# Kernel optimization log

Hardware: AMD Instinct MI355X
Metric: run time of the kernel (lower is better)

The kernel has to match this reference:

```python
import jax, jax.numpy as jnp
import numpy as np

FEAT = 1024
B = 1024
S = 64


def setup_inputs() -> dict:
    key = jax.random.key(0)
    ks = jax.random.split(key, 6)
    scale_ih = 1.0 / np.sqrt(2 * FEAT)
    scale_hh = 1.0 / np.sqrt(FEAT)
    return {
        "query": jax.random.normal(ks[0], (B, FEAT), jnp.float32) * 0.1,
        "support_context": jax.random.normal(ks[1], (S, FEAT), jnp.float32) * 0.1,
        "W_ih": jax.random.normal(ks[2], (4 * FEAT, 2 * FEAT), jnp.float32) * scale_ih,
        "W_hh": jax.random.normal(ks[3], (4 * FEAT, FEAT), jnp.float32) * scale_hh,
        "b_ih": jax.random.normal(ks[4], (4 * FEAT,), jnp.float32) * scale_hh,
        "b_hh": jax.random.normal(ks[5], (4 * FEAT,), jnp.float32) * scale_hh,
    }


def reference(query, support_context, W_ih, W_hh, b_ih, b_hh):
    # query: [B, F]; support_context: [S, F]; steps == S
    hidden = query
    cell = jnp.zeros_like(query)
    support_t = support_context.T  # [F, S]

    def step(carry, _):
        h, c = carry
        attn = jax.nn.softmax(h @ support_t, axis=1)          # [B, S]
        readout = attn @ support_context                      # [B, F]
        x = jnp.concatenate([query, readout], axis=1)         # [B, 2F]
        gates = x @ W_ih.T + b_ih + h @ W_hh.T + b_hh          # [B, 4F]
        i, f, g, o = jnp.split(gates, 4, axis=1)               # torch LSTMCell gate order
        c_new = jax.nn.sigmoid(f) * c + jax.nn.sigmoid(i) * jnp.tanh(g)
        h_new = jax.nn.sigmoid(o) * jnp.tanh(c_new) + query   # skip connection per original
        return (h_new, c_new), None

    (hidden, cell), _ = jax.lax.scan(step, (hidden, cell), None,
                                     length=support_context.shape[0])
    return hidden
```

## Files before the change

### kernel.cpp

```cpp
#include <hip/hip_runtime.h>
#include <hip/hip_bf16.h>


typedef __attribute__((ext_vector_type(8))) __bf16 bf16x8;
typedef __attribute__((ext_vector_type(4))) float f32x4;
typedef __attribute__((ext_vector_type(8))) unsigned short ushort8;

__device__ __forceinline__ ushort f2bf(float f) {
  union { float f; unsigned int u; } v; v.f = f;
  unsigned int u = v.u;
  u += 0x7FFFu + ((u >> 16) & 1u);
  return (ushort)(u >> 16);
}
__device__ __forceinline__ float bf2f(ushort u) {
  union { float f; unsigned int u; } v; v.u = ((unsigned int)u) << 16; return v.f;
}
__device__ __forceinline__ float sigm_(float x) { return 1.f / (1.f + __expf(-x)); }
__device__ __forceinline__ float tanh_(float x) {
  x = fminf(15.f, fmaxf(-15.f, x));
  float e = __expf(2.f * x);
  return (e - 1.f) / (e + 1.f);
}
__device__ __forceinline__ void async16(ushort* lds, const ushort* g) {
  __builtin_amdgcn_global_load_lds(
      (const __attribute__((address_space(1))) void*)g,
      (__attribute__((address_space(3))) void*)lds, 16, 0, 0);
}
__device__ __forceinline__ int permrow(int n) {
  int g = n >> 10, j = n & 1023;
  return ((j >> 4) << 6) | (g << 4) | (j & 15);
}

__global__ __launch_bounds__(256) void prep_kernel(
    const float* __restrict__ query, const float* __restrict__ support,
    const float* __restrict__ W_ih, const float* __restrict__ W_hh,
    const float* __restrict__ b_ih, const float* __restrict__ b_hh,
    ushort* __restrict__ Wq_bf, ushort* __restrict__ Wcomb,
    float* __restrict__ bias_p, ushort* __restrict__ X0,
    float* __restrict__ c, float* __restrict__ sT,
    ushort* __restrict__ Wr_bf, ushort* __restrict__ Sb)
{
  int g = blockIdx.x * 256 + threadIdx.x;
  int n = g >> 10, k = g & 1023;
  int np = permrow(n);
  Wq_bf[(size_t)np * 1024 + k] = f2bf(W_ih[(size_t)n * 2048 + k]);
  Wr_bf[(size_t)n * 1024 + k]  = f2bf(W_ih[(size_t)n * 2048 + 1024 + k]);
  Wcomb[(size_t)np * 1088 + k] = f2bf(W_hh[(size_t)n * 1024 + k]);
  if (g < 1024 * 1024) {
    X0[(size_t)(g >> 10) * 1088 + (g & 1023)] = f2bf(query[g]);
    c[g] = 0.f;
  }
  if (g < 4096) bias_p[permrow(g)] = b_ih[g] + b_hh[g];
  if (g < 65536) {
    int kk = g >> 6, s = g & 63;
    float v = support[(size_t)s * 1024 + kk];
    sT[g] = v;
    Sb[(size_t)s * 1024 + kk] = f2bf(v);
  }
}

__global__ __launch_bounds__(256) void sw_mfma(
    const ushort* __restrict__ Wr, const ushort* __restrict__ Sb,
    ushort* __restrict__ Wcomb)
{
  __shared__ ushort As[3][128 * 32];
  __shared__ ushort Bs[3][64 * 32];
  const int t = threadIdx.x;
  const int bm0 = blockIdx.x * 128;
  const int w = t >> 6, l = t & 63;
  const int wm = w * 32;
  const int srow = t >> 2, scol = (t & 3) * 8;
  const ushort* ga0 = Wr + (size_t)(bm0 + srow) * 1024 + scol;
  const ushort* ga1 = Wr + (size_t)(bm0 + 64 + srow) * 1024 + scol;
  const ushort* gb0 = Sb + (size_t)srow * 1024 + scol;
  const int fr = l & 15, fk = (l >> 4) * 8, fq = l >> 4;
  f32x4 acc[2][4] = {};
  const int nt = 32;
  async16(&As[0][t * 8], ga0); async16(&As[0][2048 + t * 8], ga1);
  async16(&Bs[0][t * 8], gb0);
  async16(&As[1][t * 8], ga0 + 32); async16(&As[1][2048 + t * 8], ga1 + 32);
  async16(&Bs[1][t * 8], gb0 + 32);
  for (int it = 0; it < nt; it++) {
    if (it + 1 < nt) { asm volatile("s_waitcnt vmcnt(3)" ::: "memory"); }
    else             { asm volatile("s_waitcnt vmcnt(0)" ::: "memory"); }
    __builtin_amdgcn_s_barrier();
    __builtin_amdgcn_sched_barrier(0);
    const int b = it % 3;
    const ushort* pa = &As[b][(wm + fr) * 32 + fk];
    const ushort* pb = &Bs[b][fr * 32 + fk];
    bf16x8 af[2], bfv[4];
#pragma unroll
    for (int mi = 0; mi < 2; mi++) af[mi] = *(const bf16x8*)(pa + mi * 512);
#pragma unroll
    for (int ni = 0; ni < 4; ni++) bfv[ni] = *(const bf16x8*)(pb + ni * 512);
    if (it + 2 < nt) {
      const int pbuf = (it + 2) % 3;
      const int k0 = (it + 2) << 5;
      async16(&As[pbuf][t * 8], ga0 + k0); async16(&As[pbuf][2048 + t * 8], ga1 + k0);
      async16(&Bs[pbuf][t * 8], gb0 + k0);
    }
#pragma unroll
    for (int mi = 0; mi < 2; mi++)
#pragma unroll
      for (int ni = 0; ni < 4; ni++)
        acc[mi][ni] = __builtin_amdgcn_mfma_f32_16x16x32_bf16(af[mi], bfv[ni], acc[mi][ni], 0, 0, 0);
  }
#pragma unroll
  for (int mi = 0; mi < 2; mi++)
#pragma unroll
    for (int ni = 0; ni < 4; ni++) {
      int s = ni * 16 + fr;
      int row0 = bm0 + wm + mi * 16 + fq * 4;
#pragma unroll
      for (int jj = 0; jj < 4; jj++)
        Wcomb[(size_t)permrow(row0 + jj) * 1088 + 1024 + s] = f2bf(acc[mi][ni][jj]);
    }
}

__global__ __launch_bounds__(256) void attn_kernel(
    const ushort* __restrict__ Xh, const float* __restrict__ sT,
    ushort* __restrict__ Xa)
{
  __shared__ float hs[4][1024];
  __shared__ float part[4][4][64];
  int t = threadIdx.x;
  int b0 = blockIdx.x * 4;
#pragma unroll
  for (int i = 0; i < 2; i++) {
    int r = i * 2 + (t >> 7), c8 = (t & 127) << 3;
    ushort8 v = *(const ushort8*)&Xh[(size_t)(b0 + r) * 1088 + c8];
#pragma unroll
    for (int jj = 0; jj < 8; jj++) hs[r][c8 + jj] = bf2f(v[jj]);
  }
  __syncthreads();
  int s = t & 63, q = t >> 6;
  const float* st = sT + (size_t)q * 256 * 64 + s;
  const float* hp0 = &hs[0][q * 256];
  const float* hp1 = &hs[1][q * 256];
  const float* hp2 = &hs[2][q * 256];
  const float* hp3 = &hs[3][q * 256];
  float a0 = 0.f, a1 = 0.f, a2 = 0.f, a3 = 0.f;
#pragma unroll 4
  for (int kk = 0; kk < 256; kk += 4) {
    float s0 = st[(size_t)kk * 64], s1 = st[(size_t)(kk + 1) * 64];
    float s2 = st[(size_t)(kk + 2) * 64], s3 = st[(size_t)(kk + 3) * 64];
    float4 h0 = *(const float4*)&hp0[kk];
    float4 h1 = *(const float4*)&hp1[kk];
    float4 h2 = *(const float4*)&hp2[kk];
    float4 h3 = *(const float4*)&hp3[kk];
    a0 += h0.x * s0 + h0.y * s1 + h0.z * s2 + h0.w * s3;
    a1 += h1.x * s0 + h1.y * s1 + h1.z * s2 + h1.w * s3;
    a2 += h2.x * s0 + h2.y * s1 + h2.z * s2 + h2.w * s3;
    a3 += h3.x * s0 + h3.y * s1 + h3.z * s2 + h3.w * s3;
  }
  part[q][0][s] = a0; part[q][1][s] = a1; part[q][2][s] = a2; part[q][3][s] = a3;
  __syncthreads();
  {
    int r = t >> 6, s2 = t & 63;
    float v = part[0][r][s2] + part[1][r][s2] + part[2][r][s2] + part[3][r][s2];
    float m = v;
    for (int off = 32; off; off >>= 1) m = fmaxf(m, __shfl_xor(m, off));
    float e = __expf(v - m);
    float sm = e;
    for (int off = 32; off; off >>= 1) sm += __shfl_xor(sm, off);
    Xa[(size_t)(b0 + r) * 1088 + 1024 + s2] = f2bf(e / sm);
  }
}

__global__ __launch_bounds__(256) void gemm_step(
    const ushort* __restrict__ A, const ushort* __restrict__ Bw,
    int lda, int ldb, int K,
    const float* __restrict__ base, const float* __restrict__ bias,
    float* __restrict__ Cout,
    float* __restrict__ cbuf, const float* __restrict__ query,
    ushort* __restrict__ Xout, float* __restrict__ outp)
{
  __shared__ ushort As[3][2][64 * 32];
  __shared__ ushort Bs[3][2][128 * 32];
  const int t = threadIdx.x;
  const int bid = blockIdx.x;
  const int xcd = bid & 7, idx = bid >> 3;
  const int bx = idx & 15, byy = idx >> 4;
  const int by = xcd * 4 + byy;
  const int m0 = bx * 64, n0 = by * 128;
  const int w = t >> 6, l = t & 63;
  const int wm = (w >> 1) * 32, wn = (w & 1) * 64;
  const int srow = t >> 2, scol = (t & 3) * 8;
  const ushort* ga  = A  + (size_t)(m0 + srow) * lda + scol;
  const ushort* gb0 = Bw + (size_t)(n0 + srow) * ldb + scol;
  const ushort* gb1 = Bw + (size_t)(n0 + 64 + srow) * ldb + scol;
  const int fr = l & 15, fk = (l >> 4) * 8, fq = l >> 4;
  f32x4 acc[2][4] = {};
  const int nt = K >> 6;
#define STAGE(buf, k0)                                        \
  async16(&As[buf][0][t * 8], ga + (k0));                     \
  async16(&As[buf][1][t * 8], ga + (k0) + 32);                \
  async16(&Bs[buf][0][t * 8], gb0 + (k0));                    \
  async16(&Bs[buf][0][2048 + t * 8], gb1 + (k0));             \
  async16(&Bs[buf][1][t * 8], gb0 + (k0) + 32);               \
  async16(&Bs[buf][1][2048 + t * 8], gb1 + (k0) + 32);
  STAGE(0, 0)
  STAGE(1, 64)
  for (int it = 0; it < nt; it++) {
    if (it + 1 < nt) { asm volatile("s_waitcnt vmcnt(6)" ::: "memory"); }
    else             { asm volatile("s_waitcnt vmcnt(0)" ::: "memory"); }
    __builtin_amdgcn_s_barrier();
    __builtin_amdgcn_sched_barrier(0);
    if (it + 2 < nt) {
      const int pbuf = (it + 2) % 3;
      const int k0 = (it + 2) << 6;
      STAGE(pbuf, k0)
    }
    const int b = it % 3;
#pragma unroll
    for (int kk = 0; kk < 2; kk++) {
      const ushort* pa = &As[b][kk][(wm + fr) * 32 + fk];
      const ushort* pb = &Bs[b][kk][(wn + fr) * 32 + fk];
      bf16x8 af[2], bfv[4];
#pragma unroll
      for (int mi = 0; mi < 2; mi++) af[mi] = *(const bf16x8*)(pa + mi * 512);
#pragma unroll
      for (int ni = 0; ni < 4; ni++) bfv[ni] = *(const bf16x8*)(pb + ni * 512);
      __builtin_amdgcn_s_setprio(1);
#pragma unroll
      for (int mi = 0; mi < 2; mi++)
#pragma unroll
        for (int ni = 0; ni < 4; ni++)
          acc[mi][ni] = __builtin_amdgcn_mfma_f32_16x16x32_bf16(af[mi], bfv[ni], acc[mi][ni], 0, 0, 0);
      __builtin_amdgcn_s_setprio(0);
    }
  }
#undef STAGE
  if (!base) {
#pragma unroll
    for (int mi = 0; mi < 2; mi++)
#pragma unroll
      for (int ni = 0; ni < 4; ni++) {
        int col = n0 + wn + ni * 16 + fr;
        int row0 = m0 + wm + mi * 16 + fq * 4;
        float bv = bias[col];
#pragma unroll
        for (int jj = 0; jj < 4; jj++)
          Cout[(size_t)(row0 + jj) * 4096 + col] = acc[mi][ni][jj] + bv;
      }
    return;
  }
  const int jbase = (((n0 + wn) >> 6) << 4);
  const int jcol = jbase + fr;
#pragma unroll
  for (int mi = 0; mi < 2; mi++) {
#pragma unroll
    for (int jj = 0; jj < 4; jj++) {
      int row = m0 + wm + mi * 16 + fq * 4 + jj;
      const float* bp = base + (size_t)row * 4096 + (n0 + wn);
      float gi = acc[mi][0][jj] + bp[fr];
      float gf = acc[mi][1][jj] + bp[16 + fr];
      float gg = acc[mi][2][jj] + bp[32 + fr];
      float go = acc[mi][3][jj] + bp[48 + fr];
      size_t cidx = (size_t)row * 1024 + jcol;
      float cv = cbuf[cidx];
      float cn = sigm_(gf) * cv + sigm_(gi) * tanh_(gg);
      float hn = sigm_(go) * tanh_(cn) + query[cidx];
      cbuf[cidx] = cn;
      Xout[(size_t)row * 1088 + jcol] = f2bf(hn);
      if (outp) outp[cidx] = hn;
    }
  }
}

extern "C" void kernel_launch(void* const* d_in, const int* in_sizes, int n_in,
                              void* d_out, int out_size, void* d_ws, size_t ws_size,
                              hipStream_t stream) {
  const float* query   = (const float*)d_in[0];
  const float* support = (const float*)d_in[1];
  const float* W_ih    = (const float*)d_in[2];
  const float* W_hh    = (const float*)d_in[3];
  const float* b_ih    = (const float*)d_in[4];
  const float* b_hh    = (const float*)d_in[5];
  float* out = (float*)d_out;

  char* ws = (char*)d_ws;
  size_t off = 0;
  auto alloc = [&](size_t bytes) {
    void* p = ws + off;
    off += (bytes + 255) & ~(size_t)255;
    return p;
  };
  ushort* Wq_bf  = (ushort*)alloc((size_t)4096 * 1024 * 2);
  ushort* Wcomb  = (ushort*)alloc((size_t)4096 * 1088 * 2);
  ushort* Wr_bf  = (ushort*)alloc((size_t)4096 * 1024 * 2);
  ushort* Sb     = (ushort*)alloc((size_t)64 * 1024 * 2);
  float*  bias_p = (float*) alloc((size_t)4096 * 4);
  float*  base   = (float*) alloc((size_t)1024 * 4096 * 4);
  ushort* X0     = (ushort*)alloc((size_t)1024 * 1088 * 2);
  ushort* X1     = (ushort*)alloc((size_t)1024 * 1088 * 2);
  float*  c      = (float*) alloc((size_t)1024 * 1024 * 4);
  float*  sT     = (float*) alloc((size_t)1024 * 64 * 4);

  prep_kernel<<<16384, 256, 0, stream>>>(query, support, W_ih, W_hh, b_ih, b_hh,
                                         Wq_bf, Wcomb, bias_p, X0, c, sT,
                                         Wr_bf, Sb);
  sw_mfma<<<32, 256, 0, stream>>>(Wr_bf, Sb, Wcomb);
  gemm_step<<<512, 256, 0, stream>>>(X0, Wq_bf, 1088, 1024, 1024,
                                     nullptr, bias_p, base,
                                     nullptr, nullptr, nullptr, nullptr);
  for (int step = 0; step < 64; step++) {
    ushort* Xc = (step & 1) ? X1 : X0;
    ushort* Xn = (step & 1) ? X0 : X1;
    attn_kernel<<<256, 256, 0, stream>>>(Xc, sT, Xc);
    gemm_step<<<512, 256, 0, stream>>>(Xc, Wcomb, 1088, 1088, 1088,
                                       base, nullptr, nullptr,
                                       c, query, Xn,
                                       (step == 63) ? out : nullptr);
  }
}
```

Before: 2.014 ms.

## Fuse attention scores and softmax into the per-step LSTM gate GEMM

Removes the separate attention kernel. Each gate-GEMM block now computes h·S^T with extra MFMAs while it streams h tiles, does a softmax in LDS, and applies the attention-times-(W_r·S) term as a final K=64 chunk. This cuts one launch per step and the global round trip of the attention weights. In exchange, every block recomputes the attention scores for its 64 rows, which duplicates work across the 32 column blocks. The h buffer layout also shrinks to 1024 columns.

```diff
diff --git a/kernel.cpp b/kernel.cpp
--- a/kernel.cpp
+++ b/kernel.cpp
@@ -37,8 +37,8 @@
     const float* __restrict__ b_ih, const float* __restrict__ b_hh,
     ushort* __restrict__ Wq_bf, ushort* __restrict__ Wcomb,
     float* __restrict__ bias_p, ushort* __restrict__ X0,
-    float* __restrict__ c, float* __restrict__ sT,
-    ushort* __restrict__ Wr_bf, ushort* __restrict__ Sb)
+    float* __restrict__ c, ushort* __restrict__ Wr_bf,
+    ushort* __restrict__ Sb)
 {
   int g = blockIdx.x * 256 + threadIdx.x;
   int n = g >> 10, k = g & 1023;
@@ -47,16 +47,11 @@
   Wr_bf[(size_t)n * 1024 + k]  = f2bf(W_ih[(size_t)n * 2048 + 1024 + k]);
   Wcomb[(size_t)np * 1088 + k] = f2bf(W_hh[(size_t)n * 1024 + k]);
   if (g < 1024 * 1024) {
-    X0[(size_t)(g >> 10) * 1088 + (g & 1023)] = f2bf(query[g]);
+    X0[g] = f2bf(query[g]);
     c[g] = 0.f;
   }
   if (g < 4096) bias_p[permrow(g)] = b_ih[g] + b_hh[g];
-  if (g < 65536) {
-    int kk = g >> 6, s = g & 63;
-    float v = support[(size_t)s * 1024 + kk];
-    sT[g] = v;
-    Sb[(size_t)s * 1024 + kk] = f2bf(v);
-  }
+  if (g < 65536) Sb[g] = f2bf(support[g]);
 }
 
 __global__ __launch_bounds__(256) void sw_mfma(
@@ -117,61 +112,80 @@
     }
 }
 
-__global__ __launch_bounds__(256) void attn_kernel(
-    const ushort* __restrict__ Xh, const float* __restrict__ sT,
-    ushort* __restrict__ Xa)
+__global__ __launch_bounds__(256) void gemm_base(
+    const ushort* __restrict__ A, const ushort* __restrict__ Bw,
+    const float* __restrict__ bias, float* __restrict__ Cout)
 {
-  __shared__ float hs[4][1024];
-  __shared__ float part[4][4][64];
-  int t = threadIdx.x;
-  int b0 = blockIdx.x * 4;
-#pragma unroll
-  for (int i = 0; i < 2; i++) {
-    int r = i * 2 + (t >> 7), c8 = (t & 127) << 3;
-    ushort8 v = *(const ushort8*)&Xh[(size_t)(b0 + r) * 1088 + c8];
-#pragma unroll
-    for (int jj = 0; jj < 8; jj++) hs[r][c8 + jj] = bf2f(v[jj]);
-  }
-  __syncthreads();
-  int s = t & 63, q = t >> 6;
-  const float* st = sT + (size_t)q * 256 * 64 + s;
-  const float* hp0 = &hs[0][q * 256];
-  const float* hp1 = &hs[1][q * 256];
-  const float* hp2 = &hs[2][q * 256];
-  const float* hp3 = &hs[3][q * 256];
-  float a0 = 0.f, a1 = 0.f, a2 = 0.f, a3 = 0.f;
-#pragma unroll 4
-  for (int kk = 0; kk < 256; kk += 4) {
-    float s0 = st[(size_t)kk * 64], s1 = st[(size_t)(kk + 1) * 64];
-    float s2 = st[(size_t)(kk + 2) * 64], s3 = st[(size_t)(kk + 3) * 64];
-    float4 h0 = *(const float4*)&hp0[kk];
-    float4 h1 = *(const float4*)&hp1[kk];
-    float4 h2 = *(const float4*)&hp2[kk];
-    float4 h3 = *(const float4*)&hp3[kk];
-    a0 += h0.x * s0 + h0.y * s1 + h0.z * s2 + h0.w * s3;
-    a1 += h1.x * s0 + h1.y * s1 + h1.z * s2 + h1.w * s3;
-    a2 += h2.x * s0 + h2.y * s1 + h2.z * s2 + h2.w * s3;
-    a3 += h3.x * s0 + h3.y * s1 + h3.z * s2 + h3.w * s3;
-  }
-  part[q][0][s] = a0; part[q][1][s] = a1; part[q][2][s] = a2; part[q][3][s] = a3;
-  __syncthreads();
-  {
-    int r = t >> 6, s2 = t & 63;
-    float v = part[0][r][s2] + part[1][r][s2] + part[2][r][s2] + part[3][r][s2];
-    float m = v;
-    for (int off = 32; off; off >>= 1) m = fmaxf(m, __shfl_xor(m, off));
-    float e = __expf(v - m);
-    float sm = e;
-    for (int off = 32; off; off >>= 1) sm += __shfl_xor(sm, off);
-    Xa[(size_t)(b0 + r) * 1088 + 1024 + s2] = f2bf(e / sm);
-  }
-}
-
-__global__ __launch_bounds__(256) void gemm_step(
-    const ushort* __restrict__ A, const ushort* __restrict__ Bw,
-    int lda, int ldb, int K,
-    const float* __restrict__ base, const float* __restrict__ bias,
-    float* __restrict__ Cout,
+  __shared__ ushort As[3][2][64 * 32];
+  __shared__ ushort Bs[3][2][128 * 32];
+  const int t = threadIdx.x;
+  const int bid = blockIdx.x;
+  const int xcd = bid & 7, idx = bid >> 3;
+  const int bx = idx & 15, byy = idx >> 4;
+  const int by = xcd * 4 + byy;
+  const int m0 = bx * 64, n0 = by * 128;
+  const int w = t >> 6, l = t & 63;
+  const int wm = (w >> 1) * 32, wn = (w & 1) * 64;
+  const int srow = t >> 2, scol = (t & 3) * 8;
+  const ushort* ga  = A  + (size_t)(m0 + srow) * 1024 + scol;
+  const ushort* gb0 = Bw + (size_t)(n0 + srow) * 1024 + scol;
+  const ushort* gb1 = Bw + (size_t)(n0 + 64 + srow) * 1024 + scol;
+  const int fr = l & 15, fk = (l >> 4) * 8, fq = l >> 4;
+  f32x4 acc[2][4] = {};
+  const int nt = 16;
+#define BSTAGE(buf, k0)                                       \
+  async16(&As[buf][0][t * 8], ga + (k0));                     \
+  async16(&As[buf][1][t * 8], ga + (k0) + 32);                \
+  async16(&Bs[buf][0][t * 8], gb0 + (k0));                    \
+  async16(&Bs[buf][0][2048 + t * 8], gb1 + (k0));             \
+  async16(&Bs[buf][1][t * 8], gb0 + (k0) + 32);               \
+  async16(&Bs[buf][1][2048 + t * 8], gb1 + (k0) + 32);
+  BSTAGE(0, 0)
+  BSTAGE(1, 64)
+  for (int it = 0; it < nt; it++) {
+    if (it + 1 < nt) { asm volatile("s_waitcnt vmcnt(6)" ::: "memory"); }
+    else             { asm volatile("s_waitcnt vmcnt(0)" ::: "memory"); }
+    __builtin_amdgcn_s_barrier();
+    __builtin_amdgcn_sched_barrier(0);
+    if (it + 2 < nt) { const int pb = (it + 2) % 3; const int k0 = (it + 2) << 6; BSTAGE(pb, k0) }
+    const int b = it % 3;
+#pragma unroll
+    for (int kk = 0; kk < 2; kk++) {
+      const ushort* pa = &As[b][kk][(wm + fr) * 32 + fk];
+      const ushort* pb2 = &Bs[b][kk][(wn + fr) * 32 + fk];
+      bf16x8 af[2], bfv[4];
+#pragma unroll
+      for (int mi = 0; mi < 2; mi++) af[mi] = *(const bf16x8*)(pa + mi * 512);
+#pragma unroll
+      for (int ni = 0; ni < 4; ni++) bfv[ni] = *(const bf16x8*)(pb2 + ni * 512);
+      __builtin_amdgcn_s_setprio(1);
+#pragma unroll
+      for (int mi = 0; mi < 2; mi++)
+#pragma unroll
+        for (int ni = 0; ni < 4; ni++)
+          acc[mi][ni] = __builtin_amdgcn_mfma_f32_16x16x32_bf16(af[mi], bfv[ni], acc[mi][ni], 0, 0, 0);
+      __builtin_amdgcn_s_setprio(0);
+    }
+  }
+#undef BSTAGE
+#pragma unroll
+  for (int mi = 0; mi < 2; mi++)
+#pragma unroll
+    for (int ni = 0; ni < 4; ni++) {
+      int col = n0 + wn + ni * 16 + fr;
+      int row0 = m0 + wm + mi * 16 + fq * 4;
+      float bv = bias[col];
+#pragma unroll
+      for (int jj = 0; jj < 4; jj++)
+        Cout[(size_t)(row0 + jj) * 4096 + col] = acc[mi][ni][jj] + bv;
+    }
+}
+
+__global__ __launch_bounds__(256, 2) void gemm_fused(
+    const ushort* __restrict__ A,
+    const ushort* __restrict__ Wcomb,
+    const ushort* __restrict__ Sb,
+    const float* __restrict__ base,
     float* __restrict__ cbuf, const float* __restrict__ query,
     ushort* __restrict__ Xout, float* __restrict__ outp)
 {
@@ -186,67 +200,124 @@
   const int w = t >> 6, l = t & 63;
   const int wm = (w >> 1) * 32, wn = (w & 1) * 64;
   const int srow = t >> 2, scol = (t & 3) * 8;
-  const ushort* ga  = A  + (size_t)(m0 + srow) * lda + scol;
-  const ushort* gb0 = Bw + (size_t)(n0 + srow) * ldb + scol;
-  const ushort* gb1 = Bw + (size_t)(n0 + 64 + srow) * ldb + scol;
+  const ushort* ga  = A + (size_t)(m0 + srow) * 1024 + scol;
+  const ushort* gb0 = Wcomb + (size_t)(n0 + srow) * 1088 + scol;
+  const ushort* gb1 = Wcomb + (size_t)(n0 + 64 + srow) * 1088 + scol;
   const int fr = l & 15, fk = (l >> 4) * 8, fq = l >> 4;
+  const ushort* gsb = Sb + (size_t)((w & 1) * 32 + fr) * 1024 + fk;
   f32x4 acc[2][4] = {};
-  const int nt = K >> 6;
-#define STAGE(buf, k0)                                        \
+  f32x4 lacc[2][2] = {};
+#define FSTAGE_A(buf, k0)                                     \
   async16(&As[buf][0][t * 8], ga + (k0));                     \
-  async16(&As[buf][1][t * 8], ga + (k0) + 32);                \
+  async16(&As[buf][1][t * 8], ga + (k0) + 32);
+#define FSTAGE_B(buf, k0)                                     \
   async16(&Bs[buf][0][t * 8], gb0 + (k0));                    \
   async16(&Bs[buf][0][2048 + t * 8], gb1 + (k0));             \
   async16(&Bs[buf][1][t * 8], gb0 + (k0) + 32);               \
   async16(&Bs[buf][1][2048 + t * 8], gb1 + (k0) + 32);
-  STAGE(0, 0)
-  STAGE(1, 64)
-  for (int it = 0; it < nt; it++) {
-    if (it + 1 < nt) { asm volatile("s_waitcnt vmcnt(6)" ::: "memory"); }
-    else             { asm volatile("s_waitcnt vmcnt(0)" ::: "memory"); }
+  FSTAGE_A(0, 0) FSTAGE_B(0, 0)
+  FSTAGE_A(1, 64) FSTAGE_B(1, 64)
+  asm volatile("s_waitcnt vmcnt(6)" ::: "memory");
+  for (int it = 0; it < 16; it++) {
     __builtin_amdgcn_s_barrier();
     __builtin_amdgcn_sched_barrier(0);
-    if (it + 2 < nt) {
-      const int pbuf = (it + 2) % 3;
-      const int k0 = (it + 2) << 6;
-      STAGE(pbuf, k0)
-    }
+    const int k0 = it << 6;
+    bf16x8 sb00 = *(const bf16x8*)(gsb + k0);
+    bf16x8 sb01 = *(const bf16x8*)(gsb + k0 + 32);
+    bf16x8 sb10 = *(const bf16x8*)(gsb + k0 + 16384);
+    bf16x8 sb11 = *(const bf16x8*)(gsb + k0 + 16384 + 32);
+    if (it <= 13) { const int pb = (it + 2) % 3; FSTAGE_A(pb, k0 + 128) FSTAGE_B(pb, k0 + 128) }
+    else if (it == 14) { FSTAGE_B(1, 1024) }
     const int b = it % 3;
+    bf16x8 af2[2][2];
 #pragma unroll
     for (int kk = 0; kk < 2; kk++) {
       const ushort* pa = &As[b][kk][(wm + fr) * 32 + fk];
-      const ushort* pb = &Bs[b][kk][(wn + fr) * 32 + fk];
-      bf16x8 af[2], bfv[4];
-#pragma unroll
-      for (int mi = 0; mi < 2; mi++) af[mi] = *(const bf16x8*)(pa + mi * 512);
-#pragma unroll
-      for (int ni = 0; ni < 4; ni++) bfv[ni] = *(const bf16x8*)(pb + ni * 512);
+      const ushort* pb2 = &Bs[b][kk][(wn + fr) * 32 + fk];
+      bf16x8 bfv[4];
+#pragma unroll
+      for (int mi = 0; mi < 2; mi++) af2[kk][mi] = *(const bf16x8*)(pa + mi * 512);
+#pragma unroll
+      for (int ni = 0; ni < 4; ni++) bfv[ni] = *(const bf16x8*)(pb2 + ni * 512);
       __builtin_amdgcn_s_setprio(1);
 #pragma unroll
       for (int mi = 0; mi < 2; mi++)
 #pragma unroll
         for (int ni = 0; ni < 4; ni++)
-          acc[mi][ni] = __builtin_amdgcn_mfma_f32_16x16x32_bf16(af[mi], bfv[ni], acc[mi][ni], 0, 0, 0);
+          acc[mi][ni] = __builtin_amdgcn_mfma_f32_16x16x32_bf16(af2[kk][mi], bfv[ni], acc[mi][ni], 0, 0, 0);
       __builtin_amdgcn_s_setprio(0);
     }
-  }
-#undef STAGE
-  if (!base) {
+    if (it <= 13)      { asm volatile("s_waitcnt vmcnt(6)" ::: "memory"); }
+    else if (it == 14) { asm volatile("s_waitcnt vmcnt(4)" ::: "memory"); }
+    else               { asm volatile("s_waitcnt vmcnt(0)" ::: "memory"); }
+    __builtin_amdgcn_sched_barrier(0);
+    lacc[0][0] = __builtin_amdgcn_mfma_f32_16x16x32_bf16(af2[0][0], sb00, lacc[0][0], 0, 0, 0);
+    lacc[0][1] = __builtin_amdgcn_mfma_f32_16x16x32_bf16(af2[0][0], sb10, lacc[0][1], 0, 0, 0);
+    lacc[1][0] = __builtin_amdgcn_mfma_f32_16x16x32_bf16(af2[0][1], sb00, lacc[1][0], 0, 0, 0);
+    lacc[1][1] = __builtin_amdgcn_mfma_f32_16x16x32_bf16(af2[0][1], sb10, lacc[1][1], 0, 0, 0);
+    lacc[0][0] = __builtin_amdgcn_mfma_f32_16x16x32_bf16(af2[1][0], sb01, lacc[0][0], 0, 0, 0);
+    lacc[0][1] = __builtin_amdgcn_mfma_f32_16x16x32_bf16(af2[1][0], sb11, lacc[0][1], 0, 0, 0);
+    lacc[1][0] = __builtin_amdgcn_mfma_f32_16x16x32_bf16(af2[1][1], sb01, lacc[1][0], 0, 0, 0);
+    lacc[1][1] = __builtin_amdgcn_mfma_f32_16x16x32_bf16(af2[1][1], sb11, lacc[1][1], 0, 0, 0);
+  }
+  __builtin_amdgcn_s_barrier();
+  {
+    float* lg = (float*)&Bs[0][0][0];
+    const int sbase = (w & 1) * 32;
 #pragma unroll
     for (int mi = 0; mi < 2; mi++)
 #pragma unroll
-      for (int ni = 0; ni < 4; ni++) {
-        int col = n0 + wn + ni * 16 + fr;
-        int row0 = m0 + wm + mi * 16 + fq * 4;
-        float bv = bias[col];
+      for (int ni = 0; ni < 2; ni++) {
+        int s = sbase + ni * 16 + fr;
+        int r0 = wm + mi * 16 + fq * 4;
 #pragma unroll
         for (int jj = 0; jj < 4; jj++)
-          Cout[(size_t)(row0 + jj) * 4096 + col] = acc[mi][ni][jj] + bv;
+          lg[(r0 + jj) * 64 + s] = lacc[mi][ni][jj];
       }
-    return;
-  }
-  const int jbase = (((n0 + wn) >> 6) << 4);
-  const int jcol = jbase + fr;
+  }
+  __syncthreads();
+  {
+    const int r = t >> 2, q = t & 3;
+    float* lg = (float*)&Bs[0][0][0];
+    float p[16];
+#pragma unroll
+    for (int i = 0; i < 16; i++) p[i] = lg[r * 64 + q * 16 + i];
+    float mx = p[0];
+#pragma unroll
+    for (int i = 1; i < 16; i++) mx = fmaxf(mx, p[i]);
+    mx = fmaxf(mx, __shfl_xor(mx, 1));
+    mx = fmaxf(mx, __shfl_xor(mx, 2));
+    float sm = 0.f;
+#pragma unroll
+    for (int i = 0; i < 16; i++) { p[i] = __expf(p[i] - mx); sm += p[i]; }
+    sm += __shfl_xor(sm, 1);
+    sm += __shfl_xor(sm, 2);
+    float inv = 1.f / sm;
+    ushort* at = &As[1][q >> 1][r * 32 + (q & 1) * 16];
+#pragma unroll
+    for (int i = 0; i < 16; i++) at[i] = f2bf(p[i] * inv);
+  }
+  __syncthreads();
+#pragma unroll
+  for (int kk = 0; kk < 2; kk++) {
+    const ushort* pa = &As[1][kk][(wm + fr) * 32 + fk];
+    const ushort* pb2 = &Bs[1][kk][(wn + fr) * 32 + fk];
+    bf16x8 af[2], bfv[4];
+#pragma unroll
+    for (int mi = 0; mi < 2; mi++) af[mi] = *(const bf16x8*)(pa + mi * 512);
+#pragma unroll
+    for (int ni = 0; ni < 4; ni++) bfv[ni] = *(const bf16x8*)(pb2 + ni * 512);
+    __builtin_amdgcn_s_setprio(1);
+#pragma unroll
+    for (int mi = 0; mi < 2; mi++)
+#pragma unroll
+      for (int ni = 0; ni < 4; ni++)
+        acc[mi][ni] = __builtin_amdgcn_mfma_f32_16x16x32_bf16(af[mi], bfv[ni], acc[mi][ni], 0, 0, 0);
+    __builtin_amdgcn_s_setprio(0);
+  }
+#undef FSTAGE_A
+#undef FSTAGE_B
+  const int jcol = (((n0 + wn) >> 6) << 4) + fr;
 #pragma unroll
   for (int mi = 0; mi < 2; mi++) {
 #pragma unroll
@@ -262,7 +333,7 @@
       float cn = sigm_(gf) * cv + sigm_(gi) * tanh_(gg);
       float hn = sigm_(go) * tanh_(cn) + query[cidx];
       cbuf[cidx] = cn;
-      Xout[(size_t)row * 1088 + jcol] = f2bf(hn);
+      Xout[cidx] = f2bf(hn);
       if (outp) outp[cidx] = hn;
     }
   }
@@ -292,25 +363,19 @@
   ushort* Sb     = (ushort*)alloc((size_t)64 * 1024 * 2);
   float*  bias_p = (float*) alloc((size_t)4096 * 4);
   float*  base   = (float*) alloc((size_t)1024 * 4096 * 4);
-  ushort* X0     = (ushort*)alloc((size_t)1024 * 1088 * 2);
-  ushort* X1     = (ushort*)alloc((size_t)1024 * 1088 * 2);
+  ushort* X0     = (ushort*)alloc((size_t)1024 * 1024 * 2);
+  ushort* X1     = (ushort*)alloc((size_t)1024 * 1024 * 2);
   float*  c      = (float*) alloc((size_t)1024 * 1024 * 4);
-  float*  sT     = (float*) alloc((size_t)1024 * 64 * 4);
 
   prep_kernel<<<16384, 256, 0, stream>>>(query, support, W_ih, W_hh, b_ih, b_hh,
-                                         Wq_bf, Wcomb, bias_p, X0, c, sT,
-                                         Wr_bf, Sb);
+                                         Wq_bf, Wcomb, bias_p, X0, c, Wr_bf, Sb);
   sw_mfma<<<32, 256, 0, stream>>>(Wr_bf, Sb, Wcomb);
-  gemm_step<<<512, 256, 0, stream>>>(X0, Wq_bf, 1088, 1024, 1024,
-                                     nullptr, bias_p, base,
-                                     nullptr, nullptr, nullptr, nullptr);
+  gemm_base<<<512, 256, 0, stream>>>(X0, Wq_bf, bias_p, base);
   for (int step = 0; step < 64; step++) {
     ushort* Xc = (step & 1) ? X1 : X0;
     ushort* Xn = (step & 1) ? X0 : X1;
-    attn_kernel<<<256, 256, 0, stream>>>(Xc, sT, Xc);
-    gemm_step<<<512, 256, 0, stream>>>(Xc, Wcomb, 1088, 1088, 1088,
-                                       base, nullptr, nullptr,
-                                       c, query, Xn,
-                                       (step == 63) ? out : nullptr);
-  }
-}
+    gemm_fused<<<512, 256, 0, stream>>>(Xc, Wcomb, Sb, base,
+                                        c, query, Xn,
+                                        (step == 63) ? out : nullptr);
+  }
+}
```

Measured after the change: 1.945 ms. 3.4% less time.
